# Optimization experiments

Measured on AMD Instinct MI355X. Metric: run time of the kernel, lower is better.

Reference implementation:

```python
import jax, jax.numpy as jnp
import numpy as np
import math

B, S, D, H, FF = 2, 2048, 1024, 16, 4096
E = D // H  # per-head dim = 64
LN_EPS = 1e-5


def _layernorm(x, g, b):
    m = jnp.mean(x, axis=-1, keepdims=True)
    v = jnp.var(x, axis=-1, keepdims=True)
    return (x - m) * jax.lax.rsqrt(v + LN_EPS) * g + b


def setup_inputs() -> dict:
    key = jax.random.key(0)
    ks = jax.random.split(key, 12)
    std = 0.02
    return {
        "inputs": jax.random.normal(ks[0], (B, S, D), dtype=jnp.float32),
        "ln1_g": jnp.ones((D,), jnp.float32),
        "ln1_b": jnp.zeros((D,), jnp.float32),
        # per-head q/k/v Linear(D, E) stacked along head axis: [H, D, E]
        "wq": jax.random.normal(ks[1], (H, D, E), jnp.float32) * std,
        "bq": jax.random.normal(ks[2], (H, E), jnp.float32) * std,
        "wk": jax.random.normal(ks[3], (H, D, E), jnp.float32) * std,
        "bk": jax.random.normal(ks[4], (H, E), jnp.float32) * std,
        "wv": jax.random.normal(ks[5], (H, D, E), jnp.float32) * std,
        "bv": jax.random.normal(ks[6], (H, E), jnp.float32) * std,
        "wo": jax.random.normal(ks[7], (D, D), jnp.float32) * std,
        "bo": jnp.zeros((D,), jnp.float32),
        "ln2_g": jnp.ones((D,), jnp.float32),
        "ln2_b": jnp.zeros((D,), jnp.float32),
        "w1": jax.random.normal(ks[8], (D, FF), jnp.float32) * std,
        "b1": jnp.zeros((FF,), jnp.float32),
        "w2": jax.random.normal(ks[9], (FF, D), jnp.float32) * std,
        "b2": jnp.zeros((D,), jnp.float32),
    }


def reference(inputs, ln1_g, ln1_b, wq, bq, wk, bk, wv, bv, wo, bo,
              ln2_g, ln2_b, w1, b1, w2, b2):
    d_model = inputs.shape[-1]
    scale = jnp.asarray(math.sqrt(d_model), inputs.dtype)  # NOTE: sqrt(d_model), not d_head

    x1 = _layernorm(inputs, ln1_g, ln1_b)
    # batched per-head projections (original uses H separate Linear layers)
    q = jnp.einsum('bsd,hde->bhse', x1, wq) + bq[None, :, None, :]
    k = jnp.einsum('bsd,hde->bhse', x1, wk) + bk[None, :, None, :]
    v = jnp.einsum('bsd,hde->bhse', x1, wv) + bv[None, :, None, :]

    scores = jnp.einsum('bhqe,bhke->bhqk', q, k) / scale
    # original: nn.Softmax(dim=1) on [B, S_q, S_k] -> softmax over the QUERY axis
    attn = jax.nn.softmax(scores, axis=2)
    a = jnp.einsum('bhqk,bhke->bhqe', attn, v)  # [B, H, S, E]

    # concat heads along feature dim (head 0 first)
    bsz, _, slen, _ = a.shape
    a = a.transpose(0, 2, 1, 3).reshape(bsz, slen, d_model)
    msa = a @ wo + bo

    inter = msa + inputs
    x2 = _layernorm(inter, ln2_g, ln2_b)
    mlp = jax.nn.gelu(x2 @ w1 + b1, approximate=False) @ w2 + b2
    return mlp + inter
```

## Files before the change

kernel.cpp:

```cpp
#include <hip/hip_runtime.h>
#include <hip/hip_bf16.h>

typedef unsigned short u16;
typedef __attribute__((ext_vector_type(8))) short short8;
typedef __attribute__((ext_vector_type(4))) float f32x4;
typedef __attribute__((ext_vector_type(4))) unsigned short us4;
typedef __attribute__((ext_vector_type(4))) float float4v;

#define DEV __device__ __forceinline__

DEV float b2f(u16 v){ return __uint_as_float(((unsigned)v)<<16); }
DEV u16 f2b(float f){
  unsigned u = __float_as_uint(f);
  u = u + 0x7FFFu + ((u>>16)&1u);
  return (u16)(u>>16);
}
DEV f32x4 mfma16(short8 a, short8 b, f32x4 c){
  return __builtin_amdgcn_mfma_f32_16x16x32_bf16(a, b, c, 0, 0, 0);
}
DEV void async16(const void* g, const void* l){
  __builtin_amdgcn_global_load_lds(
    (const __attribute__((address_space(1))) unsigned int*)(uintptr_t)g,
    (__attribute__((address_space(3))) unsigned int*)(unsigned int)(uintptr_t)l,
    16, 0, 0);
}

__global__ __launch_bounds__(256) void ln_k(const float* __restrict__ xin,
    const float* __restrict__ g, const float* __restrict__ bb, u16* __restrict__ y)
{
  const int row = blockIdx.x, t = threadIdx.x, l = t&63, w = t>>6;
  const float4v rr = *(const float4v*)(xin + (size_t)row*1024 + t*4);
  float v[4] = {rr[0], rr[1], rr[2], rr[3]};
  float s  = v[0]+v[1]+v[2]+v[3];
  float ss = v[0]*v[0]+v[1]*v[1]+v[2]*v[2]+v[3]*v[3];
#pragma unroll
  for (int off=32; off>=1; off>>=1){
    s  += __shfl_down(s,  off, 64);
    ss += __shfl_down(ss, off, 64);
  }
  __shared__ float rs[4], rq[4];
  if (l==0){ rs[w]=s; rq[w]=ss; }
  __syncthreads();
  const float S = rs[0]+rs[1]+rs[2]+rs[3];
  const float Q = rq[0]+rq[1]+rq[2]+rq[3];
  const float mean = S*(1.0f/1024.0f);
  const float var  = Q*(1.0f/1024.0f) - mean*mean;
  const float rstd = rsqrtf(var + 1e-5f);
  const float4v gg = *(const float4v*)(g  + t*4);
  const float4v bv = *(const float4v*)(bb + t*4);
  us4 o;
#pragma unroll
  for (int j=0;j<4;j++) o[j] = f2b((v[j]-mean)*rstd*gg[j] + bv[j]);
  *(us4*)(y + (size_t)row*1024 + t*4) = o;
}

__global__ void transpose_k(const float* __restrict__ src, u16* __restrict__ dst,
                            int ldsrc, int lddst)
{
  __shared__ u16 tile[32][33];
  const int tx = threadIdx.x & 31, ty = threadIdx.x >> 5;
  const int c0 = blockIdx.x*32, r0 = blockIdx.y*32;
#pragma unroll
  for (int i=0;i<32;i+=8) tile[ty+i][tx] = f2b(src[(size_t)(r0+ty+i)*ldsrc + c0+tx]);
  __syncthreads();
#pragma unroll
  for (int i=0;i<32;i+=8) dst[(size_t)(c0+ty+i)*lddst + r0+tx] = tile[tx][ty+i];
}

__global__ void pack_qkv_k(const float* __restrict__ wq, const float* __restrict__ wk,
                           const float* __restrict__ wv, u16* __restrict__ BT)
{
  __shared__ u16 tile[32][33];
  const int z = blockIdx.z, which = z>>4, h = z&15;
  const float* w = (which==0?wq:(which==1?wk:wv)) + (size_t)h*1024*64;
  u16* d = BT + (size_t)(which*1024 + h*64)*1024;
  const int tx = threadIdx.x & 31, ty = threadIdx.x >> 5;
  const int c0 = blockIdx.x*32, r0 = blockIdx.y*32;
#pragma unroll
  for (int i=0;i<32;i+=8) tile[ty+i][tx] = f2b(w[(size_t)(r0+ty+i)*64 + c0+tx]);
  __syncthreads();
#pragma unroll
  for (int i=0;i<32;i+=8) d[(size_t)(c0+ty+i)*1024 + r0+tx] = tile[tx][ty+i];
}

__global__ void pack_bias_k(const float* __restrict__ bq, const float* __restrict__ bk,
                            const float* __restrict__ bv, float* __restrict__ dst)
{
  const int t = blockIdx.x*256 + threadIdx.x;
  const float* s = (t < 1024) ? bq : (t < 2048 ? bk : bv);
  dst[t] = s[t & 1023];
}

__global__ __launch_bounds__(256) void inv_l(const float* __restrict__ L, float* __restrict__ invL)
{
  const int i = blockIdx.x*256 + threadIdx.x;
  invL[i] = 1.0f / (L[i] + L[i + 65536]);
}

template<int EPI, int BN>
__global__ __launch_bounds__(256) void gemm2(
    const u16* __restrict__ A, const u16* __restrict__ BT,
    const float* __restrict__ bias, const float* __restrict__ resf,
    u16* __restrict__ outb, float* __restrict__ outf,
    int K, int lda, int ldb, int ldc)
{
  constexpr int MF   = (BN==128) ? 4 : 2;
  constexpr int BISS = BN/32;
  __shared__ u16 smem[2][(128+BN)*64];
  const int t = threadIdx.x, l = t&63, w = t>>6;
  const int bn = blockIdx.x, bm = blockIdx.y;
  const int wr = (BN==128) ? (w>>1)*64 : w*32;
  const int wc = (BN==128) ? (w&1)*64  : 0;
  const int srow = t>>3;
  const int schunk = ((t&7) ^ (srow&7)) * 8;
  const u16* gA = A  + (size_t)(bm*128 + srow)*lda + schunk;
  const u16* gB = BT + (size_t)(bn*BN  + srow)*ldb + schunk;
  char* ldsA0 = (char*)&smem[0][0];
  char* ldsB0 = (char*)&smem[0][128*64];
  char* ldsA1 = (char*)&smem[1][0];
  char* ldsB1 = (char*)&smem[1][128*64];
  int colx[2];
#pragma unroll
  for (int kk=0;kk<2;kk++) colx[kk] = (kk*64 + (l>>4)*16) ^ ((l&7)<<4);
  int rowA[MF], rowB[4];
#pragma unroll
  for (int m=0;m<MF;m++) rowA[m] = (wr + m*16 + (l&15))*128;
#pragma unroll
  for (int n=0;n<4;n++)  rowB[n] = (wc + n*16 + (l&15))*128;

#define STAGE(bufA, bufB, kt)                                            \
  {                                                                      \
    _Pragma("unroll")                                                    \
    for (int i=0;i<4;i++)                                                \
      async16(gA + (kt) + (size_t)i*32*lda, (bufA) + i*4096 + t*16);     \
    _Pragma("unroll")                                                    \
    for (int i=0;i<BISS;i++)                                             \
      async16(gB + (kt) + (size_t)i*32*ldb, (bufB) + i*4096 + t*16);     \
  }

  f32x4 acc[MF][4] = {};
  STAGE(ldsA0, ldsB0, 0);
  __syncthreads();
  const int nt = K >> 6;
  int cur = 0;
  for (int ti = 0; ti < nt; ++ti){
    char* cA = cur ? ldsA1 : ldsA0;
    char* cB = cur ? ldsB1 : ldsB0;
    if (ti + 1 < nt){
      char* pA = cur ? ldsA0 : ldsA1;
      char* pB = cur ? ldsB0 : ldsB1;
      STAGE(pA, pB, (ti+1)*64);
    }
#pragma unroll
    for (int kk=0;kk<2;kk++){
      short8 af[MF], bf[4];
#pragma unroll
      for (int m=0;m<MF;m++) af[m] = *(const short8*)(cA + rowA[m] + colx[kk]);
#pragma unroll
      for (int n=0;n<4;n++)  bf[n] = *(const short8*)(cB + rowB[n] + colx[kk]);
#pragma unroll
      for (int m=0;m<MF;m++)
#pragma unroll
        for (int n=0;n<4;n++)
          acc[m][n] = mfma16(af[m], bf[n], acc[m][n]);
    }
    __syncthreads();
    cur ^= 1;
  }
#undef STAGE

  const int rowb = bm*128 + wr, colb = bn*BN + wc;
#pragma unroll
  for (int m=0;m<MF;m++)
#pragma unroll
    for (int n=0;n<4;n++){
      const int col = colb + n*16 + (l&15);
      const float bv = bias[col];
#pragma unroll
      for (int j=0;j<4;j++){
        const int row = rowb + m*16 + (l>>4)*4 + j;
        float v = acc[m][n][j] + bv;
        const size_t idx = (size_t)row*ldc + col;
        if constexpr (EPI==0)      outb[idx] = f2b(v);
        else if constexpr (EPI==1) outf[idx] = v + resf[idx];
        else                       outb[idx] = f2b(0.5f*v*(1.0f + erff(v*0.70710678118654752f)));
      }
    }
}


__global__ __launch_bounds__(256) void attn_stats(const u16* __restrict__ QKV, float* __restrict__ L)
{
  const int g = blockIdx.x;
  const int xcd = g & 7, s_ = g >> 3;
  const int bh   = xcd*4 + (s_ & 3);
  const int kblk = (s_ >> 2) & 15;
  const int part = s_ >> 6;
  const int b = bh>>4, h = bh&15;
  const u16* Qb = QKV + (size_t)b*2048*3072 + h*64;
  const u16* Kb = Qb + 1024;
  __shared__ u16 Klds[128*64];
  __shared__ float red[4][128];
  const int t = threadIdx.x, l = t&63, w = t>>6;
#pragma unroll
  for (int i=0;i<8;i++){
    const int c = t + i*256, r = c>>4, ch = c&15;
    us4 v = *(const us4*)(Kb + (size_t)(kblk*128 + r)*3072 + ch*4);
    *(us4*)((char*)Klds + ((r*128 + ch*8) ^ ((r&7)<<4))) = v;
  }
  __syncthreads();
  short8 kf[8][2];
#pragma unroll
  for (int n=0;n<8;n++){
    const int r = n*16 + (l&15);
    const int sw = (r&7)<<4;
#pragma unroll
    for (int ks=0;ks<2;ks++)
      kf[n][ks] = *(const short8*)((char*)Klds + ((r*128 + ks*64 + (l>>4)*16) ^ sw));
  }
  float Lacc[8] = {0,0,0,0,0,0,0,0};
  short8 qf[2][2], qn[2][2];
  {
    const int qb = part*1024 + w*32;
#pragma unroll
    for (int m=0;m<2;m++)
#pragma unroll
      for (int ks=0;ks<2;ks++)
        qf[m][ks] = *(const short8*)(Qb + (size_t)(qb + m*16 + (l&15))*3072 + ks*32 + (l>>4)*8);
  }
  for (int qt = 0; qt < 8; qt++){
    if (qt < 7){
      const int qb = part*1024 + (qt+1)*128 + w*32;
#pragma unroll
      for (int m=0;m<2;m++)
#pragma unroll
        for (int ks=0;ks<2;ks++)
          qn[m][ks] = *(const short8*)(Qb + (size_t)(qb + m*16 + (l&15))*3072 + ks*32 + (l>>4)*8);
    }
#pragma unroll
    for (int m=0;m<2;m++)
#pragma unroll
      for (int n=0;n<8;n++){
        f32x4 s = {};
        s = mfma16(qf[m][0], kf[n][0], s);
        s = mfma16(qf[m][1], kf[n][1], s);
#pragma unroll
        for (int j=0;j<4;j++) Lacc[n] += __expf(s[j]*0.03125f);
      }
    if (qt < 7){
#pragma unroll
      for (int m=0;m<2;m++)
#pragma unroll
        for (int ks=0;ks<2;ks++) qf[m][ks] = qn[m][ks];
    }
  }
#pragma unroll
  for (int n=0;n<8;n++){
    Lacc[n] += __shfl_xor(Lacc[n], 16, 64);
    Lacc[n] += __shfl_xor(Lacc[n], 32, 64);
  }
  if (l < 16){
#pragma unroll
    for (int n=0;n<8;n++) red[w][n*16 + l] = Lacc[n];
  }
  __syncthreads();
  if (t < 128)
    L[(size_t)part*65536 + (size_t)bh*2048 + kblk*128 + t]
        = red[0][t]+red[1][t]+red[2][t]+red[3][t];
}

__global__ __launch_bounds__(256) void attn_pv(const u16* __restrict__ QKV,
    const float* __restrict__ invL, u16* __restrict__ Aout)
{
  const int g = blockIdx.x;
  const int xcd = g & 7, s_ = g >> 3;
  const int bh = xcd*4 + (s_ & 3);
  const int qblk = s_ >> 2;
  const int b = bh>>4, h = bh&15;
  const u16* Qb = QKV + (size_t)b*2048*3072 + h*64;
  const u16* Kb = Qb + 1024;
  const u16* Vb = Qb + 2048;
  const float* iL = invL + (size_t)bh*2048;
  __shared__ u16 Klds[64*64];
  __shared__ u16 VT[64*66];
  __shared__ u16 P[64*68];
  __shared__ float iLs[64];
  const int t = threadIdx.x, l = t&63, w = t>>6;
  short8 qf[2];
#pragma unroll
  for (int ks=0;ks<2;ks++)
    qf[ks] = *(const short8*)(Qb + (size_t)(qblk*64 + w*16 + (l&15))*3072 + ks*32 + (l>>4)*8);
  int rr[4], cc[4];
#pragma unroll
  for (int i=0;i<4;i++){ const int c = t + i*256; rr[i] = c>>4; cc[i] = c&15; }
  us4 kreg[4], vreg[4];
#pragma unroll
  for (int i=0;i<4;i++){
    kreg[i] = *(const us4*)(Kb + (size_t)rr[i]*3072 + cc[i]*4);
    vreg[i] = *(const us4*)(Vb + (size_t)rr[i]*3072 + cc[i]*4);
  }
  float ilreg = (t < 64) ? iL[t] : 0.0f;
  f32x4 acc[4] = {};
  for (int kt=0; kt<2048; kt+=64){
#pragma unroll
    for (int i=0;i<4;i++)
      *(us4*)((char*)Klds + ((rr[i]*128 + cc[i]*8) ^ ((rr[i]&7)<<4))) = kreg[i];
    if (t < 64) iLs[t] = ilreg;
    __syncthreads();
#pragma unroll
    for (int i=0;i<4;i++){
#pragma unroll
      for (int jj=0;jj<4;jj++) VT[(cc[i]*4+jj)*66 + rr[i]] = vreg[i][jj];
    }
    if (kt + 64 < 2048){
      const u16* Kn = Kb + (size_t)(kt+64)*3072;
      const u16* Vn = Vb + (size_t)(kt+64)*3072;
#pragma unroll
      for (int i=0;i<4;i++){
        kreg[i] = *(const us4*)(Kn + (size_t)rr[i]*3072 + cc[i]*4);
        vreg[i] = *(const us4*)(Vn + (size_t)rr[i]*3072 + cc[i]*4);
      }
      if (t < 64) ilreg = iL[kt + 64 + t];
    }
    float il[4];
#pragma unroll
    for (int n=0;n<4;n++) il[n] = iLs[n*16 + (l&15)];
#pragma unroll
    for (int n=0;n<4;n++){
      const int r = n*16 + (l&15);
      const int sw = (r&7)<<4;
      const short8 kf0 = *(const short8*)((char*)Klds + ((r*128 +      (l>>4)*16) ^ sw));
      const short8 kf1 = *(const short8*)((char*)Klds + ((r*128 + 64 + (l>>4)*16) ^ sw));
      f32x4 s = {};
      s = mfma16(qf[0], kf0, s);
      s = mfma16(qf[1], kf1, s);
      const int prow = w*16 + (l>>4)*4;
      const int pcol = n*16 + (l&15);
#pragma unroll
      for (int j=0;j<4;j++)
        P[(prow+j)*68 + pcol] = f2b(__expf(s[j]*0.03125f) * il[n]);
    }
    __syncthreads();
#pragma unroll
    for (int kk=0;kk<2;kk++){
      const short8 af = *(const short8*)&P[(w*16 + (l&15))*68 + kk*32 + (l>>4)*8];
#pragma unroll
      for (int n=0;n<4;n++){
        const short8 bf = *(const short8*)&VT[(n*16 + (l&15))*66 + kk*32 + (l>>4)*8];
        acc[n] = mfma16(af, bf, acc[n]);
      }
    }
  }
  const int rowb = b*2048 + qblk*64 + w*16;
  const int colb = h*64;
#pragma unroll
  for (int n=0;n<4;n++)
#pragma unroll
    for (int j=0;j<4;j++){
      const int row = rowb + (l>>4)*4 + j;
      const int col = colb + n*16 + (l&15);
      Aout[(size_t)row*1024 + col] = f2b(acc[n][j]);
    }
}

extern "C" void kernel_launch(void* const* d_in, const int* in_sizes, int n_in,
                              void* d_out, int out_size, void* d_ws, size_t ws_size,
                              hipStream_t stream)
{
  const float* x    = (const float*)d_in[0];
  const float* ln1g = (const float*)d_in[1];
  const float* ln1b = (const float*)d_in[2];
  const float* wq   = (const float*)d_in[3];
  const float* bq   = (const float*)d_in[4];
  const float* wk   = (const float*)d_in[5];
  const float* bk   = (const float*)d_in[6];
  const float* wv   = (const float*)d_in[7];
  const float* bv   = (const float*)d_in[8];
  const float* wo   = (const float*)d_in[9];
  const float* bo   = (const float*)d_in[10];
  const float* ln2g = (const float*)d_in[11];
  const float* ln2b = (const float*)d_in[12];
  const float* w1   = (const float*)d_in[13];
  const float* b1   = (const float*)d_in[14];
  const float* w2   = (const float*)d_in[15];
  const float* b2   = (const float*)d_in[16];
  float* out = (float*)d_out;

  char* ws = (char*)d_ws;
  u16*   x1      = (u16*)  (ws + 0);
  u16*   QKV     = (u16*)  (ws + 8388608);
  u16*   H1      = (u16*)  (ws + 8388608);
  float* Lbuf    = (float*)(ws + 41943040);
  u16*   Aout    = (u16*)  (ws + 42467328);
  u16*   packbuf = (u16*)  (ws + 50855936);
  float* inter   = (float*)(ws + 59244544);
  float* biasqkv = (float*)(ws + 76021760);
  float* invLb   = (float*)(ws + 76038144);
  u16*   x2 = x1;

  pack_bias_k<<<12, 256, 0, stream>>>(bq, bk, bv, biasqkv);

  ln_k<<<4096, 256, 0, stream>>>(x, ln1g, ln1b, x1);
  pack_qkv_k<<<dim3(2,32,48), 256, 0, stream>>>(wq, wk, wv, packbuf);
  gemm2<0,128><<<dim3(24,32), 256, 0, stream>>>(x1, packbuf, biasqkv,
      nullptr, QKV, nullptr, 1024, 1024, 1024, 3072);

  attn_stats<<<1024, 256, 0, stream>>>(QKV, Lbuf);
  inv_l<<<256, 256, 0, stream>>>(Lbuf, invLb);
  attn_pv  <<<1024, 256, 0, stream>>>(QKV, invLb, Aout);

  transpose_k<<<dim3(32,32), 256, 0, stream>>>(wo, packbuf, 1024, 1024);
  gemm2<1,64><<<dim3(16,32), 256, 0, stream>>>(Aout, packbuf, bo,
      x, nullptr, inter, 1024, 1024, 1024, 1024);

  ln_k<<<4096, 256, 0, stream>>>(inter, ln2g, ln2b, x2);

  transpose_k<<<dim3(128,32), 256, 0, stream>>>(w1, packbuf, 4096, 1024);
  gemm2<2,128><<<dim3(32,32), 256, 0, stream>>>(x2, packbuf, b1,
      nullptr, H1, nullptr, 1024, 1024, 1024, 4096);

  transpose_k<<<dim3(32,128), 256, 0, stream>>>(w2, packbuf, 1024, 4096);
  gemm2<1,64><<<dim3(16,32), 256, 0, stream>>>(H1, packbuf, b2,
      inter, nullptr, out, 4096, 4096, 4096, 1024);
}
```

Measured before the change: 434.7 us.

## Pre-transpose V with folded inverse-L scaling into global buffer for attn_pv

Adds a vtrans kernel that transposes V per head into a [bh, E, S] global buffer and multiplies each key column by its inverse softmax normaliser. attn_pv can then load V^T tiles with vector stores into a swizzled LDS layout, and P drops its per-element invL multiply and moves to the same swizzle. This removes the scalar transposing LDS writes and the invL staging from the hot loop, at the cost of an extra kernel and an extra write and read of V in bf16. Scaling V before the bf16 round instead of scaling P slightly changes the rounding.

New measurement: 412.3 us. -5.2%, faster.

```diff
diff --git a/kernel.cpp b/kernel.cpp
--- a/kernel.cpp
+++ b/kernel.cpp
@@ -95,6 +95,27 @@
 {
   const int i = blockIdx.x*256 + threadIdx.x;
   invL[i] = 1.0f / (L[i] + L[i + 65536]);
+}
+
+__global__ __launch_bounds__(256) void vtrans(const u16* __restrict__ QKV,
+    const float* __restrict__ invL, u16* __restrict__ VTg)
+{
+  __shared__ u16 tile[32][33];
+  __shared__ float ltile[32];
+  const int t = threadIdx.x;
+  const int bh = blockIdx.z, b = bh>>4, h = bh&15;
+  const int tok0 = blockIdx.x*32, e0 = blockIdx.y*32;
+  const u16* V = QKV + (size_t)b*2048*3072 + 2048 + h*64;
+  const int tx = t&31, ty = t>>5;
+  if (t < 32) ltile[t] = invL[(size_t)bh*2048 + tok0 + t];
+#pragma unroll
+  for (int i=0;i<32;i+=8) tile[ty+i][tx] = V[(size_t)(tok0+ty+i)*3072 + e0+tx];
+  __syncthreads();
+#pragma unroll
+  for (int i=0;i<32;i+=8){
+    const float v = b2f(tile[tx][ty+i]) * ltile[tx];
+    VTg[(size_t)bh*131072 + (size_t)(e0+ty+i)*2048 + tok0+tx] = f2b(v);
+  }
 }
 
 template<int EPI, int BN>
@@ -270,7 +291,7 @@
 }
 
 __global__ __launch_bounds__(256) void attn_pv(const u16* __restrict__ QKV,
-    const float* __restrict__ invL, u16* __restrict__ Aout)
+    const u16* __restrict__ VTg, u16* __restrict__ Aout)
 {
   const int g = blockIdx.x;
   const int xcd = g & 7, s_ = g >> 3;
@@ -279,12 +300,10 @@
   const int b = bh>>4, h = bh&15;
   const u16* Qb = QKV + (size_t)b*2048*3072 + h*64;
   const u16* Kb = Qb + 1024;
-  const u16* Vb = Qb + 2048;
-  const float* iL = invL + (size_t)bh*2048;
+  const u16* Vt = VTg + (size_t)bh*131072;
   __shared__ u16 Klds[64*64];
-  __shared__ u16 VT[64*66];
-  __shared__ u16 P[64*68];
-  __shared__ float iLs[64];
+  __shared__ u16 Vlds[64*64];
+  __shared__ u16 P[64*64];
   const int t = threadIdx.x, l = t&63, w = t>>6;
   short8 qf[2];
 #pragma unroll
@@ -297,34 +316,24 @@
 #pragma unroll
   for (int i=0;i<4;i++){
     kreg[i] = *(const us4*)(Kb + (size_t)rr[i]*3072 + cc[i]*4);
-    vreg[i] = *(const us4*)(Vb + (size_t)rr[i]*3072 + cc[i]*4);
-  }
-  float ilreg = (t < 64) ? iL[t] : 0.0f;
+    vreg[i] = *(const us4*)(Vt + (size_t)rr[i]*2048 + cc[i]*4);
+  }
   f32x4 acc[4] = {};
   for (int kt=0; kt<2048; kt+=64){
 #pragma unroll
     for (int i=0;i<4;i++)
       *(us4*)((char*)Klds + ((rr[i]*128 + cc[i]*8) ^ ((rr[i]&7)<<4))) = kreg[i];
-    if (t < 64) iLs[t] = ilreg;
     __syncthreads();
 #pragma unroll
-    for (int i=0;i<4;i++){
-#pragma unroll
-      for (int jj=0;jj<4;jj++) VT[(cc[i]*4+jj)*66 + rr[i]] = vreg[i][jj];
-    }
+    for (int i=0;i<4;i++)
+      *(us4*)((char*)Vlds + ((rr[i]*128 + cc[i]*8) ^ ((rr[i]&7)<<4))) = vreg[i];
     if (kt + 64 < 2048){
-      const u16* Kn = Kb + (size_t)(kt+64)*3072;
-      const u16* Vn = Vb + (size_t)(kt+64)*3072;
 #pragma unroll
       for (int i=0;i<4;i++){
-        kreg[i] = *(const us4*)(Kn + (size_t)rr[i]*3072 + cc[i]*4);
-        vreg[i] = *(const us4*)(Vn + (size_t)rr[i]*3072 + cc[i]*4);
+        kreg[i] = *(const us4*)(Kb + (size_t)(kt+64+rr[i])*3072 + cc[i]*4);
+        vreg[i] = *(const us4*)(Vt + (size_t)rr[i]*2048 + kt+64 + cc[i]*4);
       }
-      if (t < 64) ilreg = iL[kt + 64 + t];
-    }
-    float il[4];
-#pragma unroll
-    for (int n=0;n<4;n++) il[n] = iLs[n*16 + (l&15)];
+    }
 #pragma unroll
     for (int n=0;n<4;n++){
       const int r = n*16 + (l&15);
@@ -335,18 +344,23 @@
       s = mfma16(qf[0], kf0, s);
       s = mfma16(qf[1], kf1, s);
       const int prow = w*16 + (l>>4)*4;
-      const int pcol = n*16 + (l&15);
-#pragma unroll
-      for (int j=0;j<4;j++)
-        P[(prow+j)*68 + pcol] = f2b(__expf(s[j]*0.03125f) * il[n]);
+      const int pcb  = (n*16 + (l&15))*2;
+#pragma unroll
+      for (int j=0;j<4;j++){
+        const int pr = prow + j;
+        *(u16*)((char*)P + ((pr*128 + pcb) ^ ((pr&7)<<4))) = f2b(__expf(s[j]*0.03125f));
+      }
     }
     __syncthreads();
+    const int qrow = w*16 + (l&15);
+    const int qsw  = (qrow&7)<<4;
 #pragma unroll
     for (int kk=0;kk<2;kk++){
-      const short8 af = *(const short8*)&P[(w*16 + (l&15))*68 + kk*32 + (l>>4)*8];
+      const short8 af = *(const short8*)((char*)P + ((qrow*128 + kk*64 + (l>>4)*16) ^ qsw));
 #pragma unroll
       for (int n=0;n<4;n++){
-        const short8 bf = *(const short8*)&VT[(n*16 + (l&15))*66 + kk*32 + (l>>4)*8];
+        const int rv = n*16 + (l&15);
+        const short8 bf = *(const short8*)((char*)Vlds + ((rv*128 + kk*64 + (l>>4)*16) ^ ((rv&7)<<4)));
         acc[n] = mfma16(af, bf, acc[n]);
       }
     }
@@ -396,6 +410,7 @@
   float* inter   = (float*)(ws + 59244544);
   float* biasqkv = (float*)(ws + 76021760);
   float* invLb   = (float*)(ws + 76038144);
+  u16*   VTg     = (u16*)  (ws + 76300288);
   u16*   x2 = x1;
 
   pack_bias_k<<<12, 256, 0, stream>>>(bq, bk, bv, biasqkv);
@@ -407,7 +422,8 @@
 
   attn_stats<<<1024, 256, 0, stream>>>(QKV, Lbuf);
   inv_l<<<256, 256, 0, stream>>>(Lbuf, invLb);
-  attn_pv  <<<1024, 256, 0, stream>>>(QKV, invLb, Aout);
+  vtrans<<<dim3(64,2,32), 256, 0, stream>>>(QKV, invLb, VTg);
+  attn_pv<<<1024, 256, 0, stream>>>(QKV, VTg, Aout);
 
   transpose_k<<<dim3(32,32), 256, 0, stream>>>(wo, packbuf, 1024, 1024);
   gemm2<1,64><<<dim3(16,32), 256, 0, stream>>>(Aout, packbuf, bo,
```
